# Kernel tuning notes

Hardware: AMD Instinct MI355X
Metric: run time of the kernel (lower is better)

Reference implementation:

```python
import jax, jax.numpy as jnp
import numpy as np

B, T, E, NH = 2, 1024, 512, 8


def setup_inputs() -> dict:
    key = jax.random.key(0)
    ks = jax.random.split(key, 7)
    s = 0.02
    return {
        "x": jax.random.normal(ks[0], (B, T, E), dtype=jnp.float32),
        "W_qkv": jax.random.normal(ks[1], (E, 3 * E), dtype=jnp.float32) * s,
        "b_qkv": jax.random.normal(ks[2], (3 * E,), dtype=jnp.float32) * s,
        "W_od": jax.random.normal(ks[3], (E, 2 * NH), dtype=jnp.float32) * s,
        "b_od": jax.random.normal(ks[4], (2 * NH,), dtype=jnp.float32) * s,
        "W_out": jax.random.normal(ks[5], (E, E), dtype=jnp.float32) * s,
        "b_out": jax.random.normal(ks[6], (E,), dtype=jnp.float32) * s,
        "length": T,
    }


def reference(x, W_qkv, b_qkv, W_od, b_od, W_out, b_out, length):
    b, t, e = x.shape
    nh = W_od.shape[1] // 2
    hd = e // nh
    scaling = float(hd) ** (-0.5)

    qkv = x @ W_qkv + b_qkv
    Q, K, V = jnp.split(qkv, 3, axis=-1)  # each (b, t, e)

    od = Q @ W_od + b_od  # (b, t, 2*nh)
    offset, duration = jnp.split(od, 2, axis=-1)
    offset = jnp.tanh(offset) * length
    duration = jax.nn.sigmoid(duration) * length

    qidx = jnp.arange(length, dtype=x.dtype)[None, :, None]  # (1, t, 1)
    anchor = qidx + offset  # (b, t, nh)

    # 'b t nh -> (b nh) t'
    anchor = anchor.transpose(0, 2, 1).reshape(b * nh, t)
    duration = duration.transpose(0, 2, 1).reshape(b * nh, t)

    start = anchor - duration
    end = anchor + duration
    bl = jnp.floor(start)          # left bound index
    br = jnp.ceil(end)             # right bound index
    al = jnp.floor(anchor)         # anchor left index
    ar = al + 1                    # anchor right index
    dist_al = anchor - al          # anchor_dist_l

    r = jnp.arange(length, dtype=x.dtype)[None, None, :]  # (1, 1, t)

    def pmask(idx):  # point mask (bnh, t, t), float
        return (r == idx[:, :, None]).astype(x.dtype)

    point_weight = (1.0
                    + (bl - start)[:, :, None] * pmask(bl)
                    + (end - br)[:, :, None] * pmask(br)
                    + dist_al[:, :, None] * pmask(ar)
                    + (1.0 - dist_al)[:, :, None] * pmask(al))

    attn_mask = (r < bl[:, :, None]) | (r > br[:, :, None])  # (bnh, t, t) bool

    def heads(z):  # 'b t (nh hd) -> (b nh) t hd'
        return z.reshape(b, t, nh, hd).transpose(0, 2, 1, 3).reshape(b * nh, t, hd)

    Qh, Kh, Vh = heads(Q), heads(K), heads(V)

    scores = jnp.einsum('bic,brc->bir', Qh, Kh) * scaling
    scores = scores * point_weight
    scores = jnp.where(attn_mask, jnp.asarray(-1e8, x.dtype), scores)
    attn = jax.nn.softmax(scores, axis=-1)

    out = jnp.einsum('bir,brc->bic', attn, Vh)  # (bnh, t, hd)
    out = out.reshape(b, nh, t, hd).transpose(0, 2, 1, 3).reshape(b, t, e)
    return out @ W_out + b_out
```

## Files before the change

kernel.cpp:

```cpp
#include <hip/hip_runtime.h>

typedef unsigned short ushort_t;
typedef short s16x8 __attribute__((ext_vector_type(8)));
typedef short s16x4 __attribute__((ext_vector_type(4)));
typedef float f32x4 __attribute__((ext_vector_type(4)));

#if defined(__HIP_DEVICE_COMPILE__)
#define MFMA16(a, b, c) __builtin_amdgcn_mfma_f32_16x16x16bf16_1k(a, b, c, 0, 0, 0)
#else
__device__ __host__ static inline f32x4 MFMA16(s16x4, s16x4, f32x4 c) { return c; }
#endif

#define DEVINL __device__ __forceinline__

DEVINL void gload_lds16(const void* g, void* l) {
#if defined(__HIP_DEVICE_COMPILE__)
  __builtin_amdgcn_global_load_lds((const __attribute__((address_space(1))) void*)g,
                                   (__attribute__((address_space(3))) void*)l,
                                   16, 0, 0);
#endif
}

DEVINL ushort_t f2b(float f) {
  union { float f; unsigned int u; } v; v.f = f;
  unsigned int r = (v.u + 0x7fffu + ((v.u >> 16) & 1u)) >> 16;
  return (ushort_t)r;
}

DEVINL ushort_t f2b_hw(float f) {
  union { __bf16 h; ushort_t u; } cv;
  cv.h = (__bf16)f;
  return cv.u;
}

__global__ __launch_bounds__(256) void prep_kernel(
    const float* __restrict__ Wqkv, const float* __restrict__ bq,
    const float* __restrict__ Wod, const float* __restrict__ bod,
    const float* __restrict__ Wout, const float* __restrict__ x,
    ushort_t* __restrict__ WqkvT, ushort_t* __restrict__ WoT,
    float* __restrict__ Wcomb, float* __restrict__ bcomb,
    ushort_t* __restrict__ xbf)
{
  __shared__ ushort_t tile[64 * 72];
  const int b = blockIdx.x;
  const int tid = threadIdx.x;

  if (b < 256) {
    const float* in;
    ushort_t* out;
    int N, bx, by;
    if (b < 192) { in = Wqkv; out = WqkvT; N = 1536; bx = b % 24; by = b / 24; }
    else         { in = Wout; out = WoT;   N = 512;  bx = (b - 192) % 8; by = (b - 192) / 8; }
    const int K = 512;
    const int n0 = bx * 64, k0 = by * 64;
    const int cr = tid >> 4;
    const int cc = (tid & 15) * 4;
#pragma unroll
    for (int p = 0; p < 4; p++) {
      int k = k0 + p * 16 + cr;
      float4 v = *(const float4*)(in + k * N + n0 + cc);
      ushort4 o; o.x = f2b(v.x); o.y = f2b(v.y); o.z = f2b(v.z); o.w = f2b(v.w);
      *(ushort4*)(tile + (p * 16 + cr) * 72 + cc) = o;
    }
    __syncthreads();
#pragma unroll
    for (int p = 0; p < 4; p++) {
      int n = n0 + p * 16 + cr;
      ushort4 v;
      v.x = tile[(cc + 0) * 72 + p * 16 + cr];
      v.y = tile[(cc + 1) * 72 + p * 16 + cr];
      v.z = tile[(cc + 2) * 72 + p * 16 + cr];
      v.w = tile[(cc + 3) * 72 + p * 16 + cr];
      *(ushort4*)(out + n * K + k0 + cc) = v;
    }
    return;
  }

  if (b >= 385) {
    const int base = (b - 385) * 2048 + tid * 8;
    float4 v0 = *(const float4*)(x + base);
    float4 v1 = *(const float4*)(x + base + 4);
    s16x8 o;
    o[0] = (short)f2b_hw(v0.x); o[1] = (short)f2b_hw(v0.y);
    o[2] = (short)f2b_hw(v0.z); o[3] = (short)f2b_hw(v0.w);
    o[4] = (short)f2b_hw(v1.x); o[5] = (short)f2b_hw(v1.y);
    o[6] = (short)f2b_hw(v1.z); o[7] = (short)f2b_hw(v1.w);
    *(s16x8*)(xbf + base) = o;
    return;
  }

  const int w = tid >> 6, lane = tid & 63;
  const int c = (b - 256) * 4 + w;
  if (c > 512) return;
  float a[8];
  const float* src = (c < 512) ? (Wqkv + c * 1536 + lane * 8) : (bq + lane * 8);
  float4 a0 = *(const float4*)(src);
  float4 a1 = *(const float4*)(src + 4);
  a[0]=a0.x; a[1]=a0.y; a[2]=a0.z; a[3]=a0.w;
  a[4]=a1.x; a[5]=a1.y; a[6]=a1.z; a[7]=a1.w;

  float s[16];
#pragma unroll
  for (int j = 0; j < 16; j++) s[j] = 0.f;
#pragma unroll
  for (int i = 0; i < 8; i++) {
    const float* wp = Wod + (lane * 8 + i) * 16;
#pragma unroll
    for (int j = 0; j < 16; j++) s[j] += a[i] * wp[j];
  }
#pragma unroll
  for (int mask = 1; mask < 64; mask <<= 1)
#pragma unroll
    for (int j = 0; j < 16; j++) s[j] += __shfl_xor(s[j], mask);

  if (lane < 16) {
    if (c < 512) Wcomb[c * 16 + lane] = s[lane];
    else         bcomb[lane] = s[lane] + bod[lane];
  }
}

__global__ __launch_bounds__(256) void qkv_od_kernel(
    const float* __restrict__ x, const ushort_t* __restrict__ xbf,
    const ushort_t* __restrict__ WT,
    const float* __restrict__ bqkv,
    const float* __restrict__ Wcomb, const float* __restrict__ bcomb,
    const int* __restrict__ lenp,
    ushort_t* __restrict__ Qh, ushort_t* __restrict__ Kh, ushort_t* __restrict__ VT,
    float* __restrict__ params)
{
  const int blk = blockIdx.x;
  const int tid = threadIdx.x;

  if (blk >= 384) {
    const int w = tid >> 6, lane = tid & 63;
    const int m = (blk - 384) * 4 + w;
    int li = lenp[0];
    float len = (li > 0 && li < 1048576) ? (float)li : 1024.0f;

    const float* qp = x + m * 512 + lane * 8;
    float q[8];
    float4 qa = *(const float4*)(qp);
    float4 qb = *(const float4*)(qp + 4);
    q[0]=qa.x; q[1]=qa.y; q[2]=qa.z; q[3]=qa.w;
    q[4]=qb.x; q[5]=qb.y; q[6]=qb.z; q[7]=qb.w;

    float s[16];
#pragma unroll
    for (int j = 0; j < 16; j++) s[j] = 0.f;
#pragma unroll
    for (int i = 0; i < 8; i++) {
      const float* wp = Wcomb + (lane * 8 + i) * 16;
#pragma unroll
      for (int j = 0; j < 16; j++) s[j] += q[i] * wp[j];
    }
#pragma unroll
    for (int mask = 1; mask < 64; mask <<= 1)
#pragma unroll
      for (int j = 0; j < 16; j++) s[j] += __shfl_xor(s[j], mask);

    if (lane < 8) {
      int h = lane;
      int bb = m >> 10, t = m & 1023;
      float odo = s[h] + bcomb[h];
      float odd = s[8 + h] + bcomb[8 + h];
      float offset = tanhf(odo) * len;
      float dur = len / (1.f + expf(-odd));
      float anchor = (float)t + offset;
      float start = anchor - dur, end = anchor + dur;
      float bl = floorf(start), br = ceilf(end);
      float al = floorf(anchor);
      float da = anchor - al;
      float* pp = params + ((bb * 8 + h) * 1024 + t) * 6;
      pp[0] = bl; pp[1] = br; pp[2] = al;
      pp[3] = bl - start; pp[4] = end - br; pp[5] = da;
    }
    return;
  }

  __shared__ __align__(16) ushort_t As[64 * 32];
  __shared__ __align__(16) ushort_t Bs[128 * 32];
  const int lane = tid & 63, w = tid >> 6;
  const int wr = w >> 1, wc = w & 1;
  const int quad = lane >> 4, l16 = lane & 15;
  const int bx = blk % 12, by = blk / 12;
  const int m0 = by * 64, n0 = bx * 128;

  f32x4 acc[2][4];
#pragma unroll
  for (int i = 0; i < 2; i++)
#pragma unroll
    for (int j = 0; j < 4; j++) acc[i][j] = f32x4{0.f, 0.f, 0.f, 0.f};

  const int idx = tid * 8;
  const int ra = idx >> 5, ca = idx & 31;
  const int rb1 = (idx + 2048) >> 5, cb1 = (idx + 2048) & 31;
  const int wbase = w << 10;
  char* asb  = (char*)As + wbase;
  char* bsb0 = (char*)Bs + wbase;
  char* bsb1 = (char*)Bs + 4096 + wbase;
  const ushort_t* ga  = xbf + (m0 + ra) * 512 + ca;
  const ushort_t* gb0 = WT + (n0 + ra) * 512 + ca;
  const ushort_t* gb1 = WT + (n0 + rb1) * 512 + cb1;

  for (int k0 = 0; k0 < 512; k0 += 32) {
    __syncthreads();
    gload_lds16(ga + k0, asb);
    gload_lds16(gb0 + k0, bsb0);
    gload_lds16(gb1 + k0, bsb1);
    __syncthreads();

    s16x8 af[2], bfr[4];
#pragma unroll
    for (int mt = 0; mt < 2; mt++)
      af[mt] = *(const s16x8*)(As + (wr * 32 + mt * 16 + l16) * 32 + quad * 8);
#pragma unroll
    for (int nt = 0; nt < 4; nt++)
      bfr[nt] = *(const s16x8*)(Bs + (wc * 64 + nt * 16 + l16) * 32 + quad * 8);
#pragma unroll
    for (int mt = 0; mt < 2; mt++)
#pragma unroll
      for (int nt = 0; nt < 4; nt++)
        acc[mt][nt] = __builtin_amdgcn_mfma_f32_16x16x32_bf16(af[mt], bfr[nt], acc[mt][nt], 0, 0, 0);
  }

#pragma unroll
  for (int nt = 0; nt < 4; nt++) {
    int c = n0 + wc * 64 + nt * 16 + l16;
    float bias = bqkv[c];
    int which = c >> 9;
    int e = c & 511;
    int h = e >> 6, d = e & 63;
#pragma unroll
    for (int mt = 0; mt < 2; mt++) {
      int mbase = m0 + wr * 32 + mt * 16 + quad * 4;
      int bb = mbase >> 10, t = mbase & 1023;
      int bh = bb * 8 + h;
      if (which == 2) {
        ushort4 pk;
        pk.x = f2b(acc[mt][nt][0] + bias);
        pk.y = f2b(acc[mt][nt][1] + bias);
        pk.z = f2b(acc[mt][nt][2] + bias);
        pk.w = f2b(acc[mt][nt][3] + bias);
        *(ushort4*)(VT + (bh * 64 + d) * 1024 + t) = pk;
      } else {
        ushort_t* dst = (which == 0) ? Qh : Kh;
        float sc = (which == 0) ? 0.125f : 1.0f;
#pragma unroll
        for (int rr = 0; rr < 4; rr++)
          dst[(bh * 1024 + t + rr) * 64 + d] = f2b((acc[mt][nt][rr] + bias) * sc);
      }
    }
  }
}

__global__ __launch_bounds__(512, 4) void attn_kernel(
    const ushort_t* __restrict__ Qh, const ushort_t* __restrict__ Kh,
    const ushort_t* __restrict__ VT, const float* __restrict__ params,
    ushort_t* __restrict__ Oh)
{
  constexpr int TS = 64 * 72;
  __shared__ __align__(16) ushort_t KV[4 * TS];
  __shared__ float band[16];

  const int tid = threadIdx.x;
  const int lane = tid & 63, w = tid >> 6;
  const int wq = w >> 2;
  const int wc = w & 3;
  const int quad = lane >> 4, l16 = lane & 15;
  const int bh = blockIdx.x;
  const int mrow = blockIdx.y * 32;
  const int qidx = mrow + wq * 16 + l16;

  const float* ppl = params + (bh * 1024 + qidx) * 6;
  float bl = ppl[0], br = ppl[1], al = ppl[2];
  float wl = ppl[3], wr2 = ppl[4], da = ppl[5];
  bool empty = (br < 0.f) || (bl > 1023.f);
  float lo = empty ? 0.f    : fmaxf(bl, 0.f);
  float hi = empty ? 1023.f : fminf(br, 1023.f);
#pragma unroll
  for (int mask = 1; mask < 16; mask <<= 1) {
    lo = fminf(lo, __shfl_xor(lo, mask));
    hi = fmaxf(hi, __shfl_xor(hi, mask));
  }
  if (lane == 0) { band[w * 2] = lo; band[w * 2 + 1] = hi; }
  __syncthreads();
  float blo = band[0], bhi = band[1];
#pragma unroll
  for (int i = 1; i < 8; i++) {
    blo = fminf(blo, band[i * 2]);
    bhi = fmaxf(bhi, band[i * 2 + 1]);
  }
  const int tlo = ((int)blo) >> 6, thi = ((int)bhi) >> 6;

  const ushort_t* qrow = Qh + (bh * 1024 + qidx) * 64;
  s16x4 bq[4];
#pragma unroll
  for (int i = 0; i < 4; i++)
    bq[i] = *(const s16x4*)(qrow + i * 16 + quad * 4);

  float lr = 0.f;
  f32x4 Oacc[4];
#pragma unroll
  for (int g = 0; g < 4; g++) Oacc[g] = f32x4{0.f, 0.f, 0.f, 0.f};

  const int srow = tid >> 3, sseg = (tid & 7) * 8;
  const ushort_t* kgb = Kh + (bh * 1024 + srow) * 64 + sseg;
  const ushort_t* vgb = VT + (bh * 64 + srow) * 1024 + sseg;

  s16x8 kr, vr;
  {
    const int r0 = tlo * 64;
    kr = *(const s16x8*)(kgb + r0 * 64);
    vr = *(const s16x8*)(vgb + r0);
  }
  {
    ushort_t* Kt = KV;
    ushort_t* Vt = KV + TS;
    *(s16x8*)(Kt + srow * 72 + sseg) = kr;
    *(s16x8*)(Vt + srow * 72 + sseg) = vr;
  }
  __syncthreads();

  for (int tt = tlo; tt <= thi; tt++) {
    const int p = (tt - tlo) & 1;
    ushort_t* Ktp = KV + p * 2 * TS;
    ushort_t* Vtp = KV + p * 2 * TS + TS;
    const int r0 = tt * 64;
    const bool more = (tt + 1 <= thi);

    if (more) {
      const int r1 = (tt + 1) * 64;
      kr = *(const s16x8*)(kgb + r1 * 64);
      vr = *(const s16x8*)(vgb + r1);
    }

    const ushort_t* krow = Ktp + (wc * 16 + l16) * 72;
    f32x4 z = {0.f, 0.f, 0.f, 0.f};
#pragma unroll
    for (int i = 0; i < 4; i++) {
      s16x4 ak = *(const s16x4*)(krow + i * 16 + quad * 4);
      z = MFMA16(ak, bq[i], z);
    }

    const int cbase = r0 + wc * 16;
    const float c0f = (float)cbase, c1f = c0f + 15.f;
    bool f = (bl < c0f) && (br > c1f) && ((al + 1.f < c0f) || (al > c1f));
    s16x4 pt;
    if (__all((int)f)) {
#pragma unroll
      for (int rr = 0; rr < 4; rr++) {
        float pv = __expf(z[rr]);
        lr += pv;
        pt[rr] = (short)f2b_hw(pv);
      }
    } else {
#pragma unroll
      for (int rr = 0; rr < 4; rr++) {
        float cf = (float)(cbase + quad * 4 + rr);
        float s = z[rr];
        float wgt = 1.f;
        wgt += (cf == bl) ? wl : 0.f;
        wgt += (cf == br) ? wr2 : 0.f;
        wgt += (cf == al + 1.f) ? da : 0.f;
        wgt += (cf == al) ? (1.f - da) : 0.f;
        s *= wgt;
        s = (cf < bl || cf > br) ? -30.f : s;
        float pv = __expf(s);
        lr += pv;
        pt[rr] = (short)f2b_hw(pv);
      }
    }

#pragma unroll
    for (int g = 0; g < 4; g++) {
      s16x4 av = *(const s16x4*)(Vtp + (g * 16 + l16) * 72 + wc * 16 + quad * 4);
      Oacc[g] = MFMA16(av, pt, Oacc[g]);
    }

    if (more) {
      ushort_t* Ktn = KV + (p ^ 1) * 2 * TS;
      ushort_t* Vtn = KV + (p ^ 1) * 2 * TS + TS;
      *(s16x8*)(Ktn + srow * 72 + sseg) = kr;
      *(s16x8*)(Vtn + srow * 72 + sseg) = vr;
      __syncthreads();
    }
  }

  lr += __shfl_xor(lr, 16);
  lr += __shfl_xor(lr, 32);

  __syncthreads();
  float* Om  = (float*)KV;
  float* lwf = Om + 8 * 16 * 65;
#pragma unroll
  for (int g = 0; g < 4; g++)
#pragma unroll
    for (int rr = 0; rr < 4; rr++)
      Om[(w * 16 + l16) * 65 + g * 16 + quad * 4 + rr] = Oacc[g][rr];
  if (quad == 0) lwf[w * 16 + l16] = lr;
  __syncthreads();

  const int bb = bh >> 3, h = bh & 7;
  {
    int e = tid;
#pragma unroll
    for (int it = 0; it < 4; it++, e += 512) {
      int r = e >> 6, col = e & 63;
      int p0 = (r >> 4) * 4, rl = r & 15;
      float lg = lwf[(p0 + 0) * 16 + rl] + lwf[(p0 + 1) * 16 + rl]
               + lwf[(p0 + 2) * 16 + rl] + lwf[(p0 + 3) * 16 + rl];
      float o  = Om[((p0 + 0) * 16 + rl) * 65 + col] + Om[((p0 + 1) * 16 + rl) * 65 + col]
               + Om[((p0 + 2) * 16 + rl) * 65 + col] + Om[((p0 + 3) * 16 + rl) * 65 + col];
      int t = mrow + r;
      Oh[((bb << 10) + t) * 512 + h * 64 + col] = f2b_hw(o / lg);
    }
  }
}

__global__ __launch_bounds__(256) void out_gemm_kernel(
    const ushort_t* __restrict__ Oh, const ushort_t* __restrict__ WT,
    const float* __restrict__ bout, float* __restrict__ outp)
{
  __shared__ __align__(16) ushort_t As[64 * 32];
  __shared__ __align__(16) ushort_t Bs[64 * 32];
  const int tid = threadIdx.x;
  const int lane = tid & 63, w = tid >> 6;
  const int wr = w >> 1, wc = w & 1;
  const int quad = lane >> 4, l16 = lane & 15;
  const int m0 = blockIdx.y * 64, n0 = blockIdx.x * 64;

  f32x4 acc[2][2];
#pragma unroll
  for (int i = 0; i < 2; i++)
#pragma unroll
    for (int j = 0; j < 2; j++) acc[i][j] = f32x4{0.f, 0.f, 0.f, 0.f};

  const int idx = tid * 8;
  const int ra = idx >> 5, ca = idx & 31;
  const int wbase = w << 10;
  char* asb = (char*)As + wbase;
  char* bsb = (char*)Bs + wbase;
  const ushort_t* ga = Oh + (m0 + ra) * 512 + ca;
  const ushort_t* gb = WT + (n0 + ra) * 512 + ca;

  for (int k0 = 0; k0 < 512; k0 += 32) {
    __syncthreads();
    gload_lds16(ga + k0, asb);
    gload_lds16(gb + k0, bsb);
    __syncthreads();

    s16x8 af[2], bfr[2];
#pragma unroll
    for (int mt = 0; mt < 2; mt++)
      af[mt] = *(const s16x8*)(As + (wr * 32 + mt * 16 + l16) * 32 + quad * 8);
#pragma unroll
    for (int nt = 0; nt < 2; nt++)
      bfr[nt] = *(const s16x8*)(Bs + (wc * 32 + nt * 16 + l16) * 32 + quad * 8);
#pragma unroll
    for (int mt = 0; mt < 2; mt++)
#pragma unroll
      for (int nt = 0; nt < 2; nt++)
        acc[mt][nt] = __builtin_amdgcn_mfma_f32_16x16x32_bf16(af[mt], bfr[nt], acc[mt][nt], 0, 0, 0);
  }

#pragma unroll
  for (int nt = 0; nt < 2; nt++) {
    int c = n0 + wc * 32 + nt * 16 + l16;
    float bias = bout[c];
#pragma unroll
    for (int mt = 0; mt < 2; mt++) {
#pragma unroll
      for (int rr = 0; rr < 4; rr++) {
        int m = m0 + wr * 32 + mt * 16 + quad * 4 + rr;
        outp[m * 512 + c] = acc[mt][nt][rr] + bias;
      }
    }
  }
}

extern "C" void kernel_launch(void* const* d_in, const int* in_sizes, int n_in,
                              void* d_out, int out_size, void* d_ws, size_t ws_size,
                              hipStream_t stream)
{
  const float* x    = (const float*)d_in[0];
  const float* Wqkv = (const float*)d_in[1];
  const float* bqkv = (const float*)d_in[2];
  const float* Wod  = (const float*)d_in[3];
  const float* bod  = (const float*)d_in[4];
  const float* Wout = (const float*)d_in[5];
  const float* bout = (const float*)d_in[6];
  const int* lenp   = (const int*)d_in[7];

  char* ws = (char*)d_ws;
  ushort_t* WqkvT  = (ushort_t*)(ws);
  ushort_t* WoT    = (ushort_t*)(ws + 1572864);
  ushort_t* Qh     = (ushort_t*)(ws + 4194304);
  ushort_t* Kh     = (ushort_t*)(ws + 6291456);
  ushort_t* VT     = (ushort_t*)(ws + 8388608);
  ushort_t* Oh     = (ushort_t*)(ws + 10485760);
  float*    Wcomb  = (float*)(ws + 12582912);
  float*    bcomb  = (float*)(ws + 12615680);
  float*    params = (float*)(ws + 12615744);
  ushort_t* xbf    = (ushort_t*)(ws + 13008960);

  prep_kernel<<<897, 256, 0, stream>>>(Wqkv, bqkv, Wod, bod, Wout, x,
                                       WqkvT, WoT, Wcomb, bcomb, xbf);
  qkv_od_kernel<<<896, 256, 0, stream>>>(x, xbf, WqkvT, bqkv, Wcomb, bcomb, lenp,
                                         Qh, Kh, VT, params);
  attn_kernel<<<dim3(16, 32), 512, 0, stream>>>(Qh, Kh, VT, params, Oh);
  out_gemm_kernel<<<dim3(8, 32), 256, 0, stream>>>(Oh, WoT, bout, (float*)d_out);
}
```

Measured before the change: 123.1 us.

## Use 16x16x32 MFMA for QK scores, double K-step in GEMMs, raise attn occupancy

The attention QK^T product now uses two 16x16x32 bf16 MFMAs with 8-element fragment loads instead of four 16x16x16 MFMAs. The QKV and output GEMMs load a 64-wide K slab per barrier pair instead of 32, which halves the number of synchronisations and doubles LDS use. The attention kernel's launch bound is raised from 4 to 6 blocks per CU, which pressures registers and may cause spills.

Measured after the change: 122.7 us. No clear change (-0.3%).

```diff
diff --git a/kernel.cpp b/kernel.cpp
--- a/kernel.cpp
+++ b/kernel.cpp
@@ -10,6 +10,7 @@
 #else
 __device__ __host__ static inline f32x4 MFMA16(s16x4, s16x4, f32x4 c) { return c; }
 #endif
+#define MFMA32(a, b, c) __builtin_amdgcn_mfma_f32_16x16x32_bf16(a, b, c, 0, 0, 0)
 
 #define DEVINL __device__ __forceinline__
 
@@ -177,8 +178,8 @@
     return;
   }
 
-  __shared__ __align__(16) ushort_t As[64 * 32];
-  __shared__ __align__(16) ushort_t Bs[128 * 32];
+  __shared__ __align__(16) ushort_t As[2 * 2048];
+  __shared__ __align__(16) ushort_t Bs[2 * 4096];
   const int lane = tid & 63, w = tid >> 6;
   const int wr = w >> 1, wc = w & 1;
   const int quad = lane >> 4, l16 = lane & 15;
@@ -193,34 +194,36 @@
 
   const int idx = tid * 8;
   const int ra = idx >> 5, ca = idx & 31;
-  const int rb1 = (idx + 2048) >> 5, cb1 = (idx + 2048) & 31;
   const int wbase = w << 10;
-  char* asb  = (char*)As + wbase;
-  char* bsb0 = (char*)Bs + wbase;
-  char* bsb1 = (char*)Bs + 4096 + wbase;
   const ushort_t* ga  = xbf + (m0 + ra) * 512 + ca;
   const ushort_t* gb0 = WT + (n0 + ra) * 512 + ca;
-  const ushort_t* gb1 = WT + (n0 + rb1) * 512 + cb1;
-
-  for (int k0 = 0; k0 < 512; k0 += 32) {
+  const ushort_t* gb1 = WT + (n0 + 64 + ra) * 512 + ca;
+
+  for (int k0 = 0; k0 < 512; k0 += 64) {
     __syncthreads();
-    gload_lds16(ga + k0, asb);
-    gload_lds16(gb0 + k0, bsb0);
-    gload_lds16(gb1 + k0, bsb1);
+#pragma unroll
+    for (int ks = 0; ks < 2; ks++) {
+      gload_lds16(ga  + k0 + ks * 32, (char*)As + ks * 4096 + wbase);
+      gload_lds16(gb0 + k0 + ks * 32, (char*)Bs + ks * 8192 + wbase);
+      gload_lds16(gb1 + k0 + ks * 32, (char*)Bs + ks * 8192 + 4096 + wbase);
+    }
     __syncthreads();
 
-    s16x8 af[2], bfr[4];
-#pragma unroll
-    for (int mt = 0; mt < 2; mt++)
-      af[mt] = *(const s16x8*)(As + (wr * 32 + mt * 16 + l16) * 32 + quad * 8);
-#pragma unroll
-    for (int nt = 0; nt < 4; nt++)
-      bfr[nt] = *(const s16x8*)(Bs + (wc * 64 + nt * 16 + l16) * 32 + quad * 8);
-#pragma unroll
-    for (int mt = 0; mt < 2; mt++)
+#pragma unroll
+    for (int ks = 0; ks < 2; ks++) {
+      s16x8 af[2], bfr[4];
+#pragma unroll
+      for (int mt = 0; mt < 2; mt++)
+        af[mt] = *(const s16x8*)(As + ks * 2048 + (wr * 32 + mt * 16 + l16) * 32 + quad * 8);
 #pragma unroll
       for (int nt = 0; nt < 4; nt++)
-        acc[mt][nt] = __builtin_amdgcn_mfma_f32_16x16x32_bf16(af[mt], bfr[nt], acc[mt][nt], 0, 0, 0);
+        bfr[nt] = *(const s16x8*)(Bs + ks * 4096 + (wc * 64 + nt * 16 + l16) * 32 + quad * 8);
+#pragma unroll
+      for (int mt = 0; mt < 2; mt++)
+#pragma unroll
+        for (int nt = 0; nt < 4; nt++)
+          acc[mt][nt] = MFMA32(af[mt], bfr[nt], acc[mt][nt]);
+    }
   }
 
 #pragma unroll
@@ -253,7 +256,7 @@
   }
 }
 
-__global__ __launch_bounds__(512, 4) void attn_kernel(
+__global__ __launch_bounds__(512, 6) void attn_kernel(
     const ushort_t* __restrict__ Qh, const ushort_t* __restrict__ Kh,
     const ushort_t* __restrict__ VT, const float* __restrict__ params,
     ushort_t* __restrict__ Oh)
@@ -293,10 +296,8 @@
   const int tlo = ((int)blo) >> 6, thi = ((int)bhi) >> 6;
 
   const ushort_t* qrow = Qh + (bh * 1024 + qidx) * 64;
-  s16x4 bq[4];
-#pragma unroll
-  for (int i = 0; i < 4; i++)
-    bq[i] = *(const s16x4*)(qrow + i * 16 + quad * 4);
+  s16x8 bq0 = *(const s16x8*)(qrow + quad * 8);
+  s16x8 bq1 = *(const s16x8*)(qrow + 32 + quad * 8);
 
   float lr = 0.f;
   f32x4 Oacc[4];
@@ -335,12 +336,11 @@
     }
 
     const ushort_t* krow = Ktp + (wc * 16 + l16) * 72;
+    s16x8 ak0 = *(const s16x8*)(krow + quad * 8);
+    s16x8 ak1 = *(const s16x8*)(krow + 32 + quad * 8);
     f32x4 z = {0.f, 0.f, 0.f, 0.f};
-#pragma unroll
-    for (int i = 0; i < 4; i++) {
-      s16x4 ak = *(const s16x4*)(krow + i * 16 + quad * 4);
-      z = MFMA16(ak, bq[i], z);
-    }
+    z = MFMA32(ak0, bq0, z);
+    z = MFMA32(ak1, bq1, z);
 
     const int cbase = r0 + wc * 16;
     const float c0f = (float)cbase, c1f = c0f + 15.f;
@@ -421,8 +421,8 @@
     const ushort_t* __restrict__ Oh, const ushort_t* __restrict__ WT,
     const float* __restrict__ bout, float* __restrict__ outp)
 {
-  __shared__ __align__(16) ushort_t As[64 * 32];
-  __shared__ __align__(16) ushort_t Bs[64 * 32];
+  __shared__ __align__(16) ushort_t As[2 * 2048];
+  __shared__ __align__(16) ushort_t Bs[2 * 2048];
   const int tid = threadIdx.x;
   const int lane = tid & 63, w = tid >> 6;
   const int wr = w >> 1, wc = w & 1;
@@ -438,29 +438,33 @@
   const int idx = tid * 8;
   const int ra = idx >> 5, ca = idx & 31;
   const int wbase = w << 10;
-  char* asb = (char*)As + wbase;
-  char* bsb = (char*)Bs + wbase;
   const ushort_t* ga = Oh + (m0 + ra) * 512 + ca;
   const ushort_t* gb = WT + (n0 + ra) * 512 + ca;
 
-  for (int k0 = 0; k0 < 512; k0 += 32) {
+  for (int k0 = 0; k0 < 512; k0 += 64) {
     __syncthreads();
-    gload_lds16(ga + k0, asb);
-    gload_lds16(gb + k0, bsb);
+#pragma unroll
+    for (int ks = 0; ks < 2; ks++) {
+      gload_lds16(ga + k0 + ks * 32, (char*)As + ks * 4096 + wbase);
+      gload_lds16(gb + k0 + ks * 32, (char*)Bs + ks * 4096 + wbase);
+    }
     __syncthreads();
 
-    s16x8 af[2], bfr[2];
-#pragma unroll
-    for (int mt = 0; mt < 2; mt++)
-      af[mt] = *(const s16x8*)(As + (wr * 32 + mt * 16 + l16) * 32 + quad * 8);
-#pragma unroll
-    for (int nt = 0; nt < 2; nt++)
-      bfr[nt] = *(const s16x8*)(Bs + (wc * 32 + nt * 16 + l16) * 32 + quad * 8);
-#pragma unroll
-    for (int mt = 0; mt < 2; mt++)
+#pragma unroll
+    for (int ks = 0; ks < 2; ks++) {
+      s16x8 af[2], bfr[2];
+#pragma unroll
+      for (int mt = 0; mt < 2; mt++)
+        af[mt] = *(const s16x8*)(As + ks * 2048 + (wr * 32 + mt * 16 + l16) * 32 + quad * 8);
 #pragma unroll
       for (int nt = 0; nt < 2; nt++)
-        acc[mt][nt] = __builtin_amdgcn_mfma_f32_16x16x32_bf16(af[mt], bfr[nt], acc[mt][nt], 0, 0, 0);
+        bfr[nt] = *(const s16x8*)(Bs + ks * 2048 + (wc * 32 + nt * 16 + l16) * 32 + quad * 8);
+#pragma unroll
+      for (int mt = 0; mt < 2; mt++)
+#pragma unroll
+        for (int nt = 0; nt < 2; nt++)
+          acc[mt][nt] = MFMA32(af[mt], bfr[nt], acc[mt][nt]);
+    }
   }
 
 #pragma unroll
```
